# Kernel tuning notes

Measured on AMD Instinct MI355X. Metric: run time of the kernel, lower is better.

## Reference

```python
import jax, jax.numpy as jnp
import numpy as np

NUM_HEADS = 8

def _l2norm(t, eps=1e-12):
    # F.normalize(p=2, dim=-1) with eps clamp
    n = jnp.sqrt(jnp.sum(t * t, axis=-1, keepdims=True))
    return t / jnp.maximum(n, eps)

def setup_inputs() -> dict:
    key = jax.random.key(0)
    ks = jax.random.split(key, 4)
    B, N, C = 16, 3136, 768
    x = jax.random.normal(ks[0], (B, N, C), dtype=jnp.float32)
    W_qkv = jax.random.normal(ks[1], (C, 3 * C), dtype=jnp.float32) * (1.0 / np.sqrt(C))
    temp = jnp.ones((NUM_HEADS, 1, 1), dtype=jnp.float32)
    W_proj = jax.random.normal(ks[2], (C, C), dtype=jnp.float32) * (1.0 / np.sqrt(C))
    b_proj = jnp.zeros((C,), dtype=jnp.float32)
    return {"x": x, "W_qkv": W_qkv, "temp": temp, "W_proj": W_proj, "b_proj": b_proj}

def reference(x, W_qkv, temp, W_proj, b_proj):
    B, N, C = x.shape
    h = NUM_HEADS
    d = C // h
    qkv = (x @ W_qkv).reshape(B, N, 3, h, d)
    qkv = jnp.transpose(qkv, (2, 0, 3, 1, 4))  # [3,B,h,N,d]
    q, k, v = qkv[0], qkv[1], qkv[2]           # [B,h,N,d]
    # transpose to channel-major: [B,h,d,N]
    q = jnp.swapaxes(q, -2, -1)
    k = jnp.swapaxes(k, -2, -1)
    v = jnp.swapaxes(v, -2, -1)
    q = _l2norm(q)
    k = _l2norm(k)
    # attn = k @ q^T over token dim: [B,h,d,d]
    attn = jnp.einsum('bhcn,bhen->bhce', k, q)
    attn = attn * temp  # temp broadcasts [h,1,1]
    attn = jax.nn.softmax(attn, axis=-1)
    out = jnp.einsum('bhce,bhen->bhcn', attn, v)  # [B,h,d,N]
    out = jnp.transpose(out, (0, 3, 1, 2)).reshape(B, N, C)
    return out @ W_proj + b_proj
```

## Files before the change

### kernel.cpp

```cpp
#include <hip/hip_runtime.h>

using bf16x8 = __attribute__((ext_vector_type(8))) __bf16;
using f32x4  = __attribute__((ext_vector_type(4))) float;

#define AS1 __attribute__((address_space(1)))
#define AS3 __attribute__((address_space(3)))

__device__ __forceinline__ unsigned short f2bf(float f) {
    unsigned int x = __float_as_uint(f);
    x += 0x7fffu + ((x >> 16) & 1u);
    return (unsigned short)(x >> 16);
}

__global__ void cvt_f32_bf16_kernel(const float4* __restrict__ in, ushort4* __restrict__ out, int n4) {
    int stride = gridDim.x * blockDim.x;
    for (int i = blockIdx.x * blockDim.x + threadIdx.x; i < n4; i += stride) {
        float4 v = in[i];
        ushort4 o;
        o.x = f2bf(v.x); o.y = f2bf(v.y); o.z = f2bf(v.z); o.w = f2bf(v.w);
        out[i] = o;
    }
}

__global__ void transpose_f32_bf16_kernel(const float* __restrict__ W, unsigned short* __restrict__ Wt,
                                          int K, int N) {
    __shared__ float tile[32][33];
    int n0 = blockIdx.x << 5, k0 = blockIdx.y << 5;
    int tx = threadIdx.x, ty = threadIdx.y;
#pragma unroll
    for (int i = 0; i < 32; i += 8)
        tile[ty + i][tx] = W[(size_t)(k0 + ty + i) * N + (n0 + tx)];
    __syncthreads();
#pragma unroll
    for (int i = 0; i < 32; i += 8)
        Wt[(size_t)(n0 + ty + i) * K + (k0 + tx)] = f2bf(tile[tx][ty + i]);
}

__device__ __forceinline__ void stage_tile_128x64(const unsigned short* g, int ldK,
                                                  unsigned short* lds, int tid) {
#pragma unroll
    for (int r = 0; r < 4; ++r) {
        int i = (r << 8) + tid;
        int row = i >> 3;
        int colb = (i & 7) << 4;
        int srcb = row * (ldK << 1) + (colb ^ ((row & 7) << 4));
        __builtin_amdgcn_global_load_lds(
            (AS1 unsigned int*)(unsigned long long)((const char*)g + srcb),
            (AS3 unsigned int*)((char*)lds + (i << 4)),
            16, 0, 0);
    }
}

__device__ __forceinline__ bf16x8 lds_read_swz(const unsigned short* base, int row, int kbyte) {
    int off = (row << 7) + (kbyte ^ ((row & 7) << 4));
    return *(const bf16x8*)((const char*)base + off);
}

template <int OUTMODE>
__global__ __launch_bounds__(256, 2)
void gemm_bt_kernel(const unsigned short* __restrict__ A, const unsigned short* __restrict__ Bt,
                    unsigned short* __restrict__ obf, float* __restrict__ of32,
                    const float* __restrict__ bias, int M, int N, int K) {
    __shared__ unsigned short As[128 * 64];
    __shared__ unsigned short Bs[128 * 64];
    int tid = threadIdx.x;
    int lane = tid & 63, w = tid >> 6;
    int wm = w >> 1, wn = w & 1;
    int m0 = blockIdx.y << 7, n0 = blockIdx.x << 7;
    const unsigned short* Ag = A + (size_t)m0 * K;
    const unsigned short* Bg = Bt + (size_t)n0 * K;

    f32x4 zz = {0.f, 0.f, 0.f, 0.f};
    f32x4 acc[4][4];
#pragma unroll
    for (int a = 0; a < 4; ++a)
#pragma unroll
        for (int b = 0; b < 4; ++b) acc[a][b] = zz;

    for (int kb = 0; kb < K; kb += 64) {
        stage_tile_128x64(Ag + kb, K, As, tid);
        stage_tile_128x64(Bg + kb, K, Bs, tid);
        __syncthreads();
#pragma unroll
        for (int ks = 0; ks < 2; ++ks) {
            int kbyte = (ks << 6) + ((lane >> 4) << 4);
            bf16x8 af[4], bfr[4];
#pragma unroll
            for (int f = 0; f < 4; ++f)
                af[f] = lds_read_swz(As, (wm << 6) + (f << 4) + (lane & 15), kbyte);
#pragma unroll
            for (int f = 0; f < 4; ++f)
                bfr[f] = lds_read_swz(Bs, (wn << 6) + (f << 4) + (lane & 15), kbyte);
#pragma unroll
            for (int fm = 0; fm < 4; ++fm)
#pragma unroll
                for (int fn = 0; fn < 4; ++fn)
                    acc[fm][fn] = __builtin_amdgcn_mfma_f32_16x16x32_bf16(af[fm], bfr[fn], acc[fm][fn], 0, 0, 0);
        }
        __syncthreads();
    }

    int rbase = m0 + (wm << 6) + ((lane >> 4) << 2);
    int cbase = n0 + (wn << 6) + (lane & 15);
    if (OUTMODE == 0) {
#pragma unroll
        for (int fm = 0; fm < 4; ++fm)
#pragma unroll
            for (int j = 0; j < 4; ++j) {
                size_t ro = (size_t)(rbase + (fm << 4) + j) * N;
#pragma unroll
                for (int fn = 0; fn < 4; ++fn)
                    obf[ro + cbase + (fn << 4)] = f2bf(acc[fm][fn][j]);
            }
    } else {
        float bv[4];
#pragma unroll
        for (int fn = 0; fn < 4; ++fn) bv[fn] = bias[cbase + (fn << 4)];
#pragma unroll
        for (int fm = 0; fm < 4; ++fm)
#pragma unroll
            for (int j = 0; j < 4; ++j) {
                size_t ro = (size_t)(rbase + (fm << 4) + j) * N;
#pragma unroll
                for (int fn = 0; fn < 4; ++fn)
                    of32[ro + cbase + (fn << 4)] = acc[fm][fn][j] + bv[fn];
            }
    }
}

__global__ __launch_bounds__(256)
void cov_mfma_kernel(const unsigned short* __restrict__ qkv, float* __restrict__ S,
                     float* __restrict__ qn2, float* __restrict__ kn2) {
    __shared__ unsigned short Kl[96 * 40];
    __shared__ unsigned short Ql[96 * 40];
    int bh = blockIdx.x;
    int b = bh >> 3, h = bh & 7;
    int tok0 = blockIdx.y * 448;
    int tid = threadIdx.x;
    int lane = tid & 63, w = tid >> 6;
    int wr = w & 1, wc = w >> 1;
    int rot = tid & 7;

    f32x4 zz = {0.f, 0.f, 0.f, 0.f};
    f32x4 acc[3][3];
#pragma unroll
    for (int a = 0; a < 3; ++a)
#pragma unroll
        for (int c = 0; c < 3; ++c) acc[a][c] = zz;
    float qn = 0.f, kn = 0.f;

    const uint4* qg = (const uint4*)qkv;

    for (int step = 0; step < 14; ++step) {
        int tokBase = b * 3136 + tok0 + (step << 5);
        __syncthreads();
#pragma unroll
        for (int r = 0; r < 3; ++r) {
            int idx = (r << 8) + tid;
            int isK = idx >= 384;
            int j = isK ? idx - 384 : idx;
            int tok = j / 12, c = j % 12;
            uint4 u = qg[(size_t)(tokBase + tok) * 288 + h * 12 + (isK ? 96 : 0) + c];
            unsigned short* dst = isK ? Kl : Ql;
            const unsigned short* us = (const unsigned short*)&u;
#pragma unroll
            for (int i = 0; i < 8; ++i) {
                int e = (i + rot) & 7;
                dst[(c * 8 + e) * 40 + tok] = us[e];
            }
        }
        __syncthreads();
        if (tid < 96) {
#pragma unroll
            for (int t = 0; t < 4; ++t) {
                bf16x8 v = *(const bf16x8*)((const char*)Ql + tid * 80 + (t << 4));
#pragma unroll
                for (int i = 0; i < 8; ++i) { float f = (float)v[i]; qn = fmaf(f, f, qn); }
            }
        } else if (tid >= 128 && tid < 224) {
            int c = tid - 128;
#pragma unroll
            for (int t = 0; t < 4; ++t) {
                bf16x8 v = *(const bf16x8*)((const char*)Kl + c * 80 + (t << 4));
#pragma unroll
                for (int i = 0; i < 8; ++i) { float f = (float)v[i]; kn = fmaf(f, f, kn); }
            }
        }
        int kbyte = (lane >> 4) << 4;
        bf16x8 af[3], bfv[3];
#pragma unroll
        for (int f = 0; f < 3; ++f)
            af[f] = *(const bf16x8*)((const char*)Kl + (wr * 48 + f * 16 + (lane & 15)) * 80 + kbyte);
#pragma unroll
        for (int f = 0; f < 3; ++f)
            bfv[f] = *(const bf16x8*)((const char*)Ql + (wc * 48 + f * 16 + (lane & 15)) * 80 + kbyte);
#pragma unroll
        for (int fm = 0; fm < 3; ++fm)
#pragma unroll
            for (int fn = 0; fn < 3; ++fn)
                acc[fm][fn] = __builtin_amdgcn_mfma_f32_16x16x32_bf16(af[fm], bfv[fn], acc[fm][fn], 0, 0, 0);
    }

    float* Sb = S + (size_t)bh * 9216;
    int rloc = wr * 48 + ((lane >> 4) << 2);
    int cloc = wc * 48 + (lane & 15);
#pragma unroll
    for (int fm = 0; fm < 3; ++fm)
#pragma unroll
        for (int fn = 0; fn < 3; ++fn)
#pragma unroll
            for (int j = 0; j < 4; ++j)
                atomicAdd(&Sb[(rloc + fm * 16 + j) * 96 + cloc + fn * 16], acc[fm][fn][j]);
    if (tid < 96) atomicAdd(&qn2[bh * 96 + tid], qn);
    if (tid >= 128 && tid < 224) atomicAdd(&kn2[bh * 96 + tid - 128], kn);
}

__global__ __launch_bounds__(128)
void softmax_kernel(const float* __restrict__ S, const float* __restrict__ qn2,
                    const float* __restrict__ kn2, const float* __restrict__ temp,
                    unsigned short* __restrict__ attnb) {
    int bh = blockIdx.x, h = bh & 7;
    __shared__ float Sl[96 * 97];
    __shared__ float qinv[96];
    int tid = threadIdx.x;
    const float* Sg = S + (size_t)bh * 9216;
    for (int i = tid; i < 9216; i += 128) Sl[(i / 96) * 97 + (i % 96)] = Sg[i];
    if (tid < 96) qinv[tid] = 1.f / fmaxf(sqrtf(qn2[bh * 96 + tid]), 1e-12f);
    __syncthreads();
    if (tid < 96) {
        int c = tid;
        float scale = (1.f / fmaxf(sqrtf(kn2[bh * 96 + c]), 1e-12f)) * temp[h];
        float* row = &Sl[c * 97];
        float mx = -3.4e38f;
        for (int e = 0; e < 96; ++e) {
            float v = row[e] * scale * qinv[e];
            row[e] = v;
            mx = fmaxf(mx, v);
        }
        float s = 0.f;
        for (int e = 0; e < 96; ++e) {
            float p = __expf(row[e] - mx);
            row[e] = p;
            s += p;
        }
        float inv = 1.f / s;
        unsigned short* ab = attnb + (size_t)bh * 9216 + c * 96;
        for (int e = 0; e < 96; ++e) ab[e] = f2bf(row[e] * inv);
    }
}

__global__ __launch_bounds__(256)
void attn_v_kernel(const unsigned short* __restrict__ qkv, const unsigned short* __restrict__ attnb,
                   unsigned short* __restrict__ Y) {
    int n0 = blockIdx.x << 6;
    int bh = blockIdx.y;
    int b = bh >> 3, h = bh & 7;
    __shared__ unsigned short Asm[96 * 104];
    __shared__ unsigned short Vs[64 * 104];
    int tid = threadIdx.x;
    int lane = tid & 63, w = tid >> 6;

    const unsigned int* ag = (const unsigned int*)(attnb + (size_t)bh * 9216);
#pragma unroll
    for (int r = 0; r < 18; ++r) {
        int i2 = (r << 8) + tid;
        int c = i2 / 48, ep = i2 % 48;
        *(unsigned int*)&Asm[c * 104 + (ep << 1)] = ag[i2];
    }
    size_t vbase = (size_t)(b * 3136 + n0) * 1152 + 768 + h * 48;
    const unsigned int* vg = (const unsigned int*)qkv;
#pragma unroll
    for (int r = 0; r < 12; ++r) {
        int i2 = (r << 8) + tid;
        int row = i2 / 48, ep = i2 % 48;
        *(unsigned int*)&Vs[row * 104 + (ep << 1)] = vg[vbase + (size_t)row * 1152 + ep];
    }
    __syncthreads();

    f32x4 zz = {0.f, 0.f, 0.f, 0.f};
    f32x4 acc[6];
#pragma unroll
    for (int f = 0; f < 6; ++f) acc[f] = zz;

#pragma unroll
    for (int ks = 0; ks < 3; ++ks) {
        int kbyte = (ks << 6) + ((lane >> 4) << 4);
        bf16x8 av = *(const bf16x8*)((const char*)Vs + ((w << 4) + (lane & 15)) * 208 + kbyte);
#pragma unroll
        for (int fn = 0; fn < 6; ++fn) {
            bf16x8 bv = *(const bf16x8*)((const char*)Asm + ((fn << 4) + (lane & 15)) * 208 + kbyte);
            acc[fn] = __builtin_amdgcn_mfma_f32_16x16x32_bf16(av, bv, acc[fn], 0, 0, 0);
        }
    }

    int rlocal = n0 + (w << 4) + ((lane >> 4) << 2);
#pragma unroll
    for (int fn = 0; fn < 6; ++fn)
#pragma unroll
        for (int j = 0; j < 4; ++j)
            Y[(size_t)(b * 3136 + rlocal + j) * 768 + h * 96 + (fn << 4) + (lane & 15)] = f2bf(acc[fn][j]);
}

extern "C" void kernel_launch(void* const* d_in, const int* in_sizes, int n_in,
                              void* d_out, int out_size, void* d_ws, size_t ws_size,
                              hipStream_t stream) {
    const float* x     = (const float*)d_in[0];
    const float* Wqkv  = (const float*)d_in[1];
    const float* temp  = (const float*)d_in[2];
    const float* Wproj = (const float*)d_in[3];
    const float* bproj = (const float*)d_in[4];
    float* out = (float*)d_out;
    char* ws = (char*)d_ws;

    unsigned short* xbf    = (unsigned short*)(ws);
    unsigned short* qkvbf  = (unsigned short*)(ws + 77070336);
    unsigned short* wqkvt  = (unsigned short*)(ws + 308281344);
    unsigned short* wprojt = (unsigned short*)(ws + 311820288);
    float*          Sbuf   = (float*)        (ws + 312999936);
    float*          qn2    = (float*)        (ws + 317718528);
    float*          kn2    = (float*)        (ws + 317767680);
    unsigned short* attnb  = (unsigned short*)(ws + 317816832);
    unsigned short* ybf    = xbf;

    hipMemsetAsync(Sbuf, 0, 4718592 + 49152 + 49152, stream);

    cvt_f32_bf16_kernel<<<2048, 256, 0, stream>>>((const float4*)x, (ushort4*)xbf, 38535168 / 4);
    transpose_f32_bf16_kernel<<<dim3(72, 24), dim3(32, 8), 0, stream>>>(Wqkv, wqkvt, 768, 2304);
    transpose_f32_bf16_kernel<<<dim3(24, 24), dim3(32, 8), 0, stream>>>(Wproj, wprojt, 768, 768);

    gemm_bt_kernel<0><<<dim3(18, 392), 256, 0, stream>>>(xbf, wqkvt, qkvbf, nullptr, nullptr,
                                                         50176, 2304, 768);
    cov_mfma_kernel<<<dim3(128, 7), 256, 0, stream>>>(qkvbf, Sbuf, qn2, kn2);
    softmax_kernel<<<128, 128, 0, stream>>>(Sbuf, qn2, kn2, temp, attnb);
    attn_v_kernel<<<dim3(49, 128), 256, 0, stream>>>(qkvbf, attnb, ybf);
    gemm_bt_kernel<1><<<dim3(6, 392), 256, 0, stream>>>(ybf, wprojt, nullptr, out, bproj,
                                                        50176, 768, 768);
}
```

Before: 451.9 us.

## Rewrite GEMMs as 256x256 tiles with triple-buffered async LDS pipeline

```diff
diff --git a/kernel.cpp b/kernel.cpp
--- a/kernel.cpp
+++ b/kernel.cpp
@@ -36,75 +36,100 @@
         Wt[(size_t)(n0 + ty + i) * K + (k0 + tx)] = f2bf(tile[tx][ty + i]);
 }
 
-__device__ __forceinline__ void stage_tile_128x64(const unsigned short* g, int ldK,
-                                                  unsigned short* lds, int tid) {
-#pragma unroll
-    for (int r = 0; r < 4; ++r) {
-        int i = (r << 8) + tid;
-        int row = i >> 3;
-        int colb = (i & 7) << 4;
-        int srcb = row * (ldK << 1) + (colb ^ ((row & 7) << 4));
-        __builtin_amdgcn_global_load_lds(
-            (AS1 unsigned int*)(unsigned long long)((const char*)g + srcb),
-            (AS3 unsigned int*)((char*)lds + (i << 4)),
-            16, 0, 0);
-    }
-}
-
-__device__ __forceinline__ bf16x8 lds_read_swz(const unsigned short* base, int row, int kbyte) {
-    int off = (row << 7) + (kbyte ^ ((row & 7) << 4));
-    return *(const bf16x8*)((const char*)base + off);
+__device__ __forceinline__ void stage32(const unsigned short* Ag, const unsigned short* Bg,
+                                        int kb, int K, char* buf, int tid) {
+#pragma unroll
+    for (int r = 0; r < 2; ++r) {
+        int i = (r << 9) + tid;
+        int row = i >> 2, slot = i & 3;
+        int srcb = row * (K << 1) + (kb << 1) + ((slot ^ (row & 3)) << 4);
+        __builtin_amdgcn_global_load_lds((AS1 unsigned int*)((const char*)Ag + srcb),
+                                         (AS3 unsigned int*)(buf + (i << 4)), 16, 0, 0);
+    }
+#pragma unroll
+    for (int r = 0; r < 2; ++r) {
+        int i = (r << 9) + tid;
+        int row = i >> 2, slot = i & 3;
+        int srcb = row * (K << 1) + (kb << 1) + ((slot ^ (row & 3)) << 4);
+        __builtin_amdgcn_global_load_lds((AS1 unsigned int*)((const char*)Bg + srcb),
+                                         (AS3 unsigned int*)(buf + 16384 + (i << 4)), 16, 0, 0);
+    }
+}
+
+__device__ __forceinline__ bf16x8 rdfrag(const char* base, int row, int lane) {
+    int off = (row << 6) + (((lane >> 4) << 4) ^ ((row & 3) << 4));
+    return *(const bf16x8*)(base + off);
 }
 
 template <int OUTMODE>
-__global__ __launch_bounds__(256, 2)
-void gemm_bt_kernel(const unsigned short* __restrict__ A, const unsigned short* __restrict__ Bt,
+__global__ __launch_bounds__(512, 2)
+void gemm256_kernel(const unsigned short* __restrict__ A, const unsigned short* __restrict__ Bt,
                     unsigned short* __restrict__ obf, float* __restrict__ of32,
-                    const float* __restrict__ bias, int M, int N, int K) {
-    __shared__ unsigned short As[128 * 64];
-    __shared__ unsigned short Bs[128 * 64];
-    int tid = threadIdx.x;
-    int lane = tid & 63, w = tid >> 6;
-    int wm = w >> 1, wn = w & 1;
-    int m0 = blockIdx.y << 7, n0 = blockIdx.x << 7;
+                    const float* __restrict__ bias, int M, int N, int K, int ntx) {
+    __shared__ char smem[3 * 32768];
+    int tid = threadIdx.x, lane = tid & 63, w = tid >> 6;
+    int wm = w >> 2, wn = w & 3;
+
+    int nwg = gridDim.x;
+    int q = nwg >> 3, r = nwg & 7;
+    int orig = blockIdx.x;
+    int xcd = orig & 7, lin = orig >> 3;
+    int wg = (xcd < r ? xcd * (q + 1) : r * (q + 1) + (xcd - r) * q) + lin;
+    int by = wg / ntx, bx = wg - by * ntx;
+    int m0 = by << 8, n0 = bx << 8;
     const unsigned short* Ag = A + (size_t)m0 * K;
     const unsigned short* Bg = Bt + (size_t)n0 * K;
+    int nkt = K >> 5;
 
     f32x4 zz = {0.f, 0.f, 0.f, 0.f};
-    f32x4 acc[4][4];
-#pragma unroll
-    for (int a = 0; a < 4; ++a)
+    f32x4 acc[8][4];
+#pragma unroll
+    for (int a = 0; a < 8; ++a)
 #pragma unroll
         for (int b = 0; b < 4; ++b) acc[a][b] = zz;
 
-    for (int kb = 0; kb < K; kb += 64) {
-        stage_tile_128x64(Ag + kb, K, As, tid);
-        stage_tile_128x64(Bg + kb, K, Bs, tid);
-        __syncthreads();
-#pragma unroll
-        for (int ks = 0; ks < 2; ++ks) {
-            int kbyte = (ks << 6) + ((lane >> 4) << 4);
-            bf16x8 af[4], bfr[4];
-#pragma unroll
-            for (int f = 0; f < 4; ++f)
-                af[f] = lds_read_swz(As, (wm << 6) + (f << 4) + (lane & 15), kbyte);
-#pragma unroll
-            for (int f = 0; f < 4; ++f)
-                bfr[f] = lds_read_swz(Bs, (wn << 6) + (f << 4) + (lane & 15), kbyte);
-#pragma unroll
-            for (int fm = 0; fm < 4; ++fm)
-#pragma unroll
-                for (int fn = 0; fn < 4; ++fn)
-                    acc[fm][fn] = __builtin_amdgcn_mfma_f32_16x16x32_bf16(af[fm], bfr[fn], acc[fm][fn], 0, 0, 0);
-        }
-        __syncthreads();
-    }
-
-    int rbase = m0 + (wm << 6) + ((lane >> 4) << 2);
+    stage32(Ag, Bg, 0, K, smem, tid);
+    stage32(Ag, Bg, 32, K, smem + 32768, tid);
+
+    for (int t = 0; t < nkt; ++t) {
+        int p = t % 3;
+        char* Ab = smem + p * 32768;
+        char* Bb = Ab + 16384;
+        if (t + 2 < nkt) stage32(Ag, Bg, (t + 2) << 5, K, smem + ((t + 2) % 3) * 32768, tid);
+        if (t + 3 <= nkt)      asm volatile("s_waitcnt vmcnt(8)" ::: "memory");
+        else if (t + 2 == nkt) asm volatile("s_waitcnt vmcnt(4)" ::: "memory");
+        else                   asm volatile("s_waitcnt vmcnt(0)" ::: "memory");
+        asm volatile("s_barrier" ::: "memory");
+
+        bf16x8 bfr[4], af[8];
+#pragma unroll
+        for (int f = 0; f < 4; ++f) bfr[f] = rdfrag(Bb, (wn << 6) + (f << 4) + (lane & 15), lane);
+#pragma unroll
+        for (int f = 0; f < 8; ++f) af[f] = rdfrag(Ab, (wm << 7) + (f << 4) + (lane & 15), lane);
+
+        __builtin_amdgcn_s_setprio(1);
+#pragma unroll
+        for (int fm = 0; fm < 4; ++fm)
+#pragma unroll
+            for (int fn = 0; fn < 4; ++fn)
+                acc[fm][fn] = __builtin_amdgcn_mfma_f32_16x16x32_bf16(af[fm], bfr[fn], acc[fm][fn], 0, 0, 0);
+        __builtin_amdgcn_s_setprio(0);
+        asm volatile("s_barrier" ::: "memory");
+        __builtin_amdgcn_s_setprio(1);
+#pragma unroll
+        for (int fm = 4; fm < 8; ++fm)
+#pragma unroll
+            for (int fn = 0; fn < 4; ++fn)
+                acc[fm][fn] = __builtin_amdgcn_mfma_f32_16x16x32_bf16(af[fm], bfr[fn], acc[fm][fn], 0, 0, 0);
+        __builtin_amdgcn_s_setprio(0);
+        asm volatile("s_barrier" ::: "memory");
+    }
+
+    int rbase = m0 + (wm << 7) + ((lane >> 4) << 2);
     int cbase = n0 + (wn << 6) + (lane & 15);
     if (OUTMODE == 0) {
 #pragma unroll
-        for (int fm = 0; fm < 4; ++fm)
+        for (int fm = 0; fm < 8; ++fm)
 #pragma unroll
             for (int j = 0; j < 4; ++j) {
                 size_t ro = (size_t)(rbase + (fm << 4) + j) * N;
@@ -117,7 +142,7 @@
 #pragma unroll
         for (int fn = 0; fn < 4; ++fn) bv[fn] = bias[cbase + (fn << 4)];
 #pragma unroll
-        for (int fm = 0; fm < 4; ++fm)
+        for (int fm = 0; fm < 8; ++fm)
 #pragma unroll
             for (int j = 0; j < 4; ++j) {
                 size_t ro = (size_t)(rbase + (fm << 4) + j) * N;
@@ -328,11 +353,11 @@
     transpose_f32_bf16_kernel<<<dim3(72, 24), dim3(32, 8), 0, stream>>>(Wqkv, wqkvt, 768, 2304);
     transpose_f32_bf16_kernel<<<dim3(24, 24), dim3(32, 8), 0, stream>>>(Wproj, wprojt, 768, 768);
 
-    gemm_bt_kernel<0><<<dim3(18, 392), 256, 0, stream>>>(xbf, wqkvt, qkvbf, nullptr, nullptr,
-                                                         50176, 2304, 768);
+    gemm256_kernel<0><<<196 * 9, 512, 0, stream>>>(xbf, wqkvt, qkvbf, nullptr, nullptr,
+                                                   50176, 2304, 768, 9);
     cov_mfma_kernel<<<dim3(128, 7), 256, 0, stream>>>(qkvbf, Sbuf, qn2, kn2);
     softmax_kernel<<<128, 128, 0, stream>>>(Sbuf, qn2, kn2, temp, attnb);
     attn_v_kernel<<<dim3(49, 128), 256, 0, stream>>>(qkvbf, attnb, ybf);
-    gemm_bt_kernel<1><<<dim3(6, 392), 256, 0, stream>>>(ybf, wprojt, nullptr, out, bproj,
-                                                        50176, 768, 768);
-}
+    gemm256_kernel<1><<<196 * 3, 512, 0, stream>>>(ybf, wprojt, nullptr, out, bproj,
+                                                   50176, 768, 768, 3);
+}
```

New measurement: 492.2 us. 8.9% more time.

## Fold attention matrix into projection weights per batch and add XCD remapping

Applied to the files above, without the earlier changes.

```diff
diff --git a/kernel.cpp b/kernel.cpp
--- a/kernel.cpp
+++ b/kernel.cpp
@@ -10,6 +10,12 @@
     unsigned int x = __float_as_uint(f);
     x += 0x7fffu + ((x >> 16) & 1u);
     return (unsigned short)(x >> 16);
+}
+
+__device__ __forceinline__ int xcd_remap(int orig, int nwg) {
+    int q = nwg >> 3, r = nwg & 7;
+    int xcd = orig & 7, lin = orig >> 3;
+    return (xcd < r ? xcd * (q + 1) : r * (q + 1) + (xcd - r) * q) + lin;
 }
 
 __global__ void cvt_f32_bf16_kernel(const float4* __restrict__ in, ushort4* __restrict__ out, int n4) {
@@ -56,17 +62,17 @@
     return *(const bf16x8*)((const char*)base + off);
 }
 
-template <int OUTMODE>
 __global__ __launch_bounds__(256, 2)
 void gemm_bt_kernel(const unsigned short* __restrict__ A, const unsigned short* __restrict__ Bt,
-                    unsigned short* __restrict__ obf, float* __restrict__ of32,
-                    const float* __restrict__ bias, int M, int N, int K) {
+                    unsigned short* __restrict__ obf, int M, int N, int K, int ntx) {
     __shared__ unsigned short As[128 * 64];
     __shared__ unsigned short Bs[128 * 64];
     int tid = threadIdx.x;
     int lane = tid & 63, w = tid >> 6;
     int wm = w >> 1, wn = w & 1;
-    int m0 = blockIdx.y << 7, n0 = blockIdx.x << 7;
+    int wg = xcd_remap(blockIdx.x, gridDim.x);
+    int bx = wg % ntx, by = wg / ntx;
+    int m0 = by << 7, n0 = bx << 7;
     const unsigned short* Ag = A + (size_t)m0 * K;
     const unsigned short* Bg = Bt + (size_t)n0 * K;
 
@@ -102,30 +108,89 @@
 
     int rbase = m0 + (wm << 6) + ((lane >> 4) << 2);
     int cbase = n0 + (wn << 6) + (lane & 15);
-    if (OUTMODE == 0) {
-#pragma unroll
-        for (int fm = 0; fm < 4; ++fm)
-#pragma unroll
-            for (int j = 0; j < 4; ++j) {
-                size_t ro = (size_t)(rbase + (fm << 4) + j) * N;
+#pragma unroll
+    for (int fm = 0; fm < 4; ++fm)
+#pragma unroll
+        for (int j = 0; j < 4; ++j) {
+            size_t ro = (size_t)(rbase + (fm << 4) + j) * N;
+#pragma unroll
+            for (int fn = 0; fn < 4; ++fn)
+                obf[ro + cbase + (fn << 4)] = f2bf(acc[fm][fn][j]);
+        }
+}
+
+__global__ __launch_bounds__(256, 2)
+void gemm_v_proj_kernel(const unsigned short* __restrict__ qkv, const unsigned short* __restrict__ MT,
+                        float* __restrict__ out, const float* __restrict__ bias) {
+    __shared__ unsigned short As[128 * 64];
+    __shared__ unsigned short Bs[128 * 64];
+    int tid = threadIdx.x;
+    int lane = tid & 63, w = tid >> 6;
+    int wm = w >> 1, wn = w & 1;
+    int wg = xcd_remap(blockIdx.x, gridDim.x);
+    int bx = wg % 6;
+    int t2 = wg / 6;
+    int mt = t2 % 25, b = t2 / 25;
+    int m0 = mt << 7, n0 = bx << 7;
+    const unsigned short* Ab = qkv + (size_t)b * 3136 * 2304 + 1536;
+    const unsigned short* Bg = MT + (size_t)b * 589824 + (size_t)n0 * 768;
+
+    f32x4 zz = {0.f, 0.f, 0.f, 0.f};
+    f32x4 acc[4][4];
+#pragma unroll
+    for (int a = 0; a < 4; ++a)
+#pragma unroll
+        for (int c = 0; c < 4; ++c) acc[a][c] = zz;
+
+    for (int kb = 0; kb < 768; kb += 64) {
+#pragma unroll
+        for (int r = 0; r < 4; ++r) {
+            int i = (r << 8) + tid;
+            int row = i >> 3, slot = i & 7;
+            int rg = m0 + row; if (rg > 3135) rg = 3135;
+            const char* src = (const char*)(Ab + (size_t)rg * 2304 + kb) + ((slot ^ (row & 7)) << 4);
+            __builtin_amdgcn_global_load_lds(
+                (AS1 unsigned int*)(unsigned long long)src,
+                (AS3 unsigned int*)((char*)As + (i << 4)), 16, 0, 0);
+        }
+        stage_tile_128x64(Bg + kb, 768, Bs, tid);
+        __syncthreads();
+#pragma unroll
+        for (int ks = 0; ks < 2; ++ks) {
+            int kbyte = (ks << 6) + ((lane >> 4) << 4);
+            bf16x8 af[4], bfr[4];
+#pragma unroll
+            for (int f = 0; f < 4; ++f)
+                af[f] = lds_read_swz(As, (wm << 6) + (f << 4) + (lane & 15), kbyte);
+#pragma unroll
+            for (int f = 0; f < 4; ++f)
+                bfr[f] = lds_read_swz(Bs, (wn << 6) + (f << 4) + (lane & 15), kbyte);
+#pragma unroll
+            for (int fm = 0; fm < 4; ++fm)
 #pragma unroll
                 for (int fn = 0; fn < 4; ++fn)
-                    obf[ro + cbase + (fn << 4)] = f2bf(acc[fm][fn][j]);
+                    acc[fm][fn] = __builtin_amdgcn_mfma_f32_16x16x32_bf16(af[fm], bfr[fn], acc[fm][fn], 0, 0, 0);
+        }
+        __syncthreads();
+    }
+
+    int rloc = m0 + (wm << 6) + ((lane >> 4) << 2);
+    int cbase = n0 + (wn << 6) + (lane & 15);
+    float bv[4];
+#pragma unroll
+    for (int fn = 0; fn < 4; ++fn) bv[fn] = bias[cbase + (fn << 4)];
+#pragma unroll
+    for (int fm = 0; fm < 4; ++fm)
+#pragma unroll
+        for (int j = 0; j < 4; ++j) {
+            int rr = rloc + (fm << 4) + j;
+            if (rr < 3136) {
+                size_t ro = ((size_t)b * 3136 + rr) * 768;
+#pragma unroll
+                for (int fn = 0; fn < 4; ++fn)
+                    out[ro + cbase + (fn << 4)] = acc[fm][fn][j] + bv[fn];
             }
-    } else {
-        float bv[4];
-#pragma unroll
-        for (int fn = 0; fn < 4; ++fn) bv[fn] = bias[cbase + (fn << 4)];
-#pragma unroll
-        for (int fm = 0; fm < 4; ++fm)
-#pragma unroll
-            for (int j = 0; j < 4; ++j) {
-                size_t ro = (size_t)(rbase + (fm << 4) + j) * N;
-#pragma unroll
-                for (int fn = 0; fn < 4; ++fn)
-                    of32[ro + cbase + (fn << 4)] = acc[fm][fn][j] + bv[fn];
-            }
-    }
+        }
 }
 
 __global__ __launch_bounds__(256)
@@ -218,7 +283,7 @@
 __global__ __launch_bounds__(128)
 void softmax_kernel(const float* __restrict__ S, const float* __restrict__ qn2,
                     const float* __restrict__ kn2, const float* __restrict__ temp,
-                    unsigned short* __restrict__ attnb) {
+                    unsigned short* __restrict__ attnT) {
     int bh = blockIdx.x, h = bh & 7;
     __shared__ float Sl[96 * 97];
     __shared__ float qinv[96];
@@ -244,61 +309,55 @@
             s += p;
         }
         float inv = 1.f / s;
-        unsigned short* ab = attnb + (size_t)bh * 9216 + c * 96;
-        for (int e = 0; e < 96; ++e) ab[e] = f2bf(row[e] * inv);
+        unsigned short* ab = attnT + (size_t)bh * 9216;
+        for (int e = 0; e < 96; ++e) ab[e * 96 + c] = f2bf(row[e] * inv);
     }
 }
 
 __global__ __launch_bounds__(256)
-void attn_v_kernel(const unsigned short* __restrict__ qkv, const unsigned short* __restrict__ attnb,
-                   unsigned short* __restrict__ Y) {
-    int n0 = blockIdx.x << 6;
-    int bh = blockIdx.y;
+void attn_M_kernel(const unsigned short* __restrict__ attnT, const unsigned short* __restrict__ wprojt,
+                   unsigned short* __restrict__ MT) {
+    int bh = blockIdx.x >> 2, oc = blockIdx.x & 3;
     int b = bh >> 3, h = bh & 7;
-    __shared__ unsigned short Asm[96 * 104];
-    __shared__ unsigned short Vs[64 * 104];
-    int tid = threadIdx.x;
-    int lane = tid & 63, w = tid >> 6;
-
-    const unsigned int* ag = (const unsigned int*)(attnb + (size_t)bh * 9216);
-#pragma unroll
-    for (int r = 0; r < 18; ++r) {
-        int i2 = (r << 8) + tid;
-        int c = i2 / 48, ep = i2 % 48;
-        *(unsigned int*)&Asm[c * 104 + (ep << 1)] = ag[i2];
-    }
-    size_t vbase = (size_t)(b * 3136 + n0) * 1152 + 768 + h * 48;
-    const unsigned int* vg = (const unsigned int*)qkv;
-#pragma unroll
-    for (int r = 0; r < 12; ++r) {
-        int i2 = (r << 8) + tid;
-        int row = i2 / 48, ep = i2 % 48;
-        *(unsigned int*)&Vs[row * 104 + (ep << 1)] = vg[vbase + (size_t)row * 1152 + ep];
-    }
-    __syncthreads();
+    int tid = threadIdx.x, lane = tid & 63, w = tid >> 6;
+    int o0 = oc * 192 + w * 48;
+    const unsigned short* At = attnT + (size_t)bh * 9216;
 
     f32x4 zz = {0.f, 0.f, 0.f, 0.f};
-    f32x4 acc[6];
-#pragma unroll
-    for (int f = 0; f < 6; ++f) acc[f] = zz;
+    f32x4 acc[6][3];
+#pragma unroll
+    for (int f = 0; f < 6; ++f)
+#pragma unroll
+        for (int g = 0; g < 3; ++g) acc[f][g] = zz;
 
 #pragma unroll
     for (int ks = 0; ks < 3; ++ks) {
-        int kbyte = (ks << 6) + ((lane >> 4) << 4);
-        bf16x8 av = *(const bf16x8*)((const char*)Vs + ((w << 4) + (lane & 15)) * 208 + kbyte);
-#pragma unroll
-        for (int fn = 0; fn < 6; ++fn) {
-            bf16x8 bv = *(const bf16x8*)((const char*)Asm + ((fn << 4) + (lane & 15)) * 208 + kbyte);
-            acc[fn] = __builtin_amdgcn_mfma_f32_16x16x32_bf16(av, bv, acc[fn], 0, 0, 0);
-        }
-    }
-
-    int rlocal = n0 + (w << 4) + ((lane >> 4) << 2);
-#pragma unroll
-    for (int fn = 0; fn < 6; ++fn)
-#pragma unroll
-        for (int j = 0; j < 4; ++j)
-            Y[(size_t)(b * 3136 + rlocal + j) * 768 + h * 96 + (fn << 4) + (lane & 15)] = f2bf(acc[fn][j]);
+        int koff = ks * 32 + ((lane >> 4) << 3);
+        bf16x8 a[6], bb[3];
+#pragma unroll
+        for (int f = 0; f < 6; ++f)
+            a[f] = *(const bf16x8*)(At + (size_t)(f * 16 + (lane & 15)) * 96 + koff);
+#pragma unroll
+        for (int g = 0; g < 3; ++g)
+            bb[g] = *(const bf16x8*)(wprojt + (size_t)(o0 + g * 16 + (lane & 15)) * 768 + h * 96 + koff);
+#pragma unroll
+        for (int f = 0; f < 6; ++f)
+#pragma unroll
+            for (int g = 0; g < 3; ++g)
+                acc[f][g] = __builtin_amdgcn_mfma_f32_16x16x32_bf16(a[f], bb[g], acc[f][g], 0, 0, 0);
+    }
+
+#pragma unroll
+    for (int f = 0; f < 6; ++f)
+#pragma unroll
+        for (int g = 0; g < 3; ++g) {
+            int e = f * 16 + ((lane >> 4) << 2);
+            int o = o0 + g * 16 + (lane & 15);
+            ushort4 pk;
+            pk.x = f2bf(acc[f][g][0]); pk.y = f2bf(acc[f][g][1]);
+            pk.z = f2bf(acc[f][g][2]); pk.w = f2bf(acc[f][g][3]);
+            *(ushort4*)&MT[((size_t)b * 768 + o) * 768 + h * 96 + e] = pk;
+        }
 }
 
 extern "C" void kernel_launch(void* const* d_in, const int* in_sizes, int n_in,
@@ -319,8 +378,8 @@
     float*          Sbuf   = (float*)        (ws + 312999936);
     float*          qn2    = (float*)        (ws + 317718528);
     float*          kn2    = (float*)        (ws + 317767680);
-    unsigned short* attnb  = (unsigned short*)(ws + 317816832);
-    unsigned short* ybf    = xbf;
+    unsigned short* attnT  = (unsigned short*)(ws + 317816832);
+    unsigned short* MT     = xbf;
 
     hipMemsetAsync(Sbuf, 0, 4718592 + 49152 + 49152, stream);
 
@@ -328,11 +387,9 @@
     transpose_f32_bf16_kernel<<<dim3(72, 24), dim3(32, 8), 0, stream>>>(Wqkv, wqkvt, 768, 2304);
     transpose_f32_bf16_kernel<<<dim3(24, 24), dim3(32, 8), 0, stream>>>(Wproj, wprojt, 768, 768);
 
-    gemm_bt_kernel<0><<<dim3(18, 392), 256, 0, stream>>>(xbf, wqkvt, qkvbf, nullptr, nullptr,
-                                                         50176, 2304, 768);
+    gemm_bt_kernel<<<392 * 18, 256, 0, stream>>>(xbf, wqkvt, qkvbf, 50176, 2304, 768, 18);
     cov_mfma_kernel<<<dim3(128, 7), 256, 0, stream>>>(qkvbf, Sbuf, qn2, kn2);
-    softmax_kernel<<<128, 128, 0, stream>>>(Sbuf, qn2, kn2, temp, attnb);
-    attn_v_kernel<<<dim3(49, 128), 256, 0, stream>>>(qkvbf, attnb, ybf);
-    gemm_bt_kernel<1><<<dim3(6, 392), 256, 0, stream>>>(ybf, wprojt, nullptr, out, bproj,
-                                                        50176, 768, 768);
-}
+    softmax_kernel<<<128, 128, 0, stream>>>(Sbuf, qn2, kn2, temp, attnT);
+    attn_M_kernel<<<512, 256, 0, stream>>>(attnT, wprojt, MT);
+    gemm_v_proj_kernel<<<2400, 256, 0, stream>>>(qkvbf, MT, out, bproj);
+}
```

New measurement: 412.8 us. 8.6% less time.
